# Optimization experiments

Measured on AMD Instinct MI355X. Metric: run time of the kernel, lower is better.

Reference implementation:

```python
import jax, jax.numpy as jnp
import numpy as np

K = 16          # NUM_PARTS (foreground parts); K+1 prototypes incl. background
D = 768         # EMBED_DIM
C = 200         # NUM_CLASSES
LN_EPS = 1e-6


def setup_inputs() -> dict:
    key = jax.random.key(0)
    k1, k2, k3, k4 = jax.random.split(key, 4)
    B, H, W = 32, 24, 24
    patch_features = jax.random.normal(k1, (B, H, W, D), dtype=jnp.float32)
    prototypes = 0.02 * jax.random.normal(k2, (K + 1, D), dtype=jnp.float32)
    ln_gamma = jnp.ones((D,), dtype=jnp.float32)
    ln_beta = jnp.zeros((D,), dtype=jnp.float32)
    # keras Dense default: glorot_uniform kernel, zero bias
    lim = np.sqrt(6.0 / (D + C)).astype(np.float32)
    w_cls = jax.random.uniform(k3, (D, C), dtype=jnp.float32, minval=-lim, maxval=lim)
    b_cls = jnp.zeros((C,), dtype=jnp.float32)
    return {
        "patch_features": patch_features,
        "prototypes": prototypes,
        "ln_gamma": ln_gamma,
        "ln_beta": ln_beta,
        "w_cls": w_cls,
        "b_cls": b_cls,
    }


def reference(patch_features, prototypes, ln_gamma, ln_beta, w_cls, b_cls):
    B, H, W, Dm = patch_features.shape
    P = H * W
    x = patch_features.reshape(B, P, Dm)                      # (B,P,D)

    # squared euclidean distance to K+1 prototypes, expressed as a GEMM:
    # ||z - p||^2 = ||z||^2 - 2 z.p + ||p||^2   -> (B,P,K+1)
    x_sq = jnp.sum(x * x, axis=-1, keepdims=True)             # (B,P,1)
    p_sq = jnp.sum(prototypes * prototypes, axis=-1)          # (K+1,)
    xp = jnp.einsum("bpd,kd->bpk", x, prototypes)             # (B,P,K+1)
    dists = x_sq - 2.0 * xp + p_sq                            # (B,P,K+1)

    # eval path: plain softmax over -distances
    a = jax.nn.softmax(-dists, axis=-1)                       # (B,P,K+1)

    # attention maps (B, K+1, H, W)
    A = jnp.transpose(a, (0, 2, 1)).reshape(B, K + 1, H, W)

    # weighted aggregation of patch features per part, normalized by P
    v_all = jnp.einsum("bpk,bpd->bkd", a, x) / jnp.float32(P) # (B,K+1,D)
    v_fg = v_all[:, :K, :]                                    # (B,K,D)

    # layernorm over last axis (eps=1e-6, learnable gamma/beta)
    mu = jnp.mean(v_fg, axis=-1, keepdims=True)
    var = jnp.mean(jnp.square(v_fg - mu), axis=-1, keepdims=True)
    v_norm = (v_fg - mu) * jax.lax.rsqrt(var + LN_EPS) * ln_gamma + ln_beta

    # shared per-part classifier + mean aggregation over parts
    logits_parts = jnp.einsum("bkd,dc->bkc", v_norm, w_cls) + b_cls  # (B,K,C)
    logits_agg = jnp.mean(logits_parts, axis=1)                      # (B,C)

    return (A, v_norm, logits_parts, logits_agg)
```

## Files before the change

### kernel.cpp

```cpp
#include <hip/hip_runtime.h>
#include <hip/hip_bf16.h>

#define B    32
#define P    576
#define D    768
#define K1   17
#define KFG  16
#define C    200
#define LN_EPS 1e-6f

typedef __attribute__((ext_vector_type(8))) short short8;
typedef __attribute__((ext_vector_type(4))) float f32x4;

__device__ inline short8 cvt8(float4 a, float4 b) {
    union { unsigned u[4]; short8 s; } r;
    union { __hip_bfloat162 h; unsigned u; } c;
    c.h = __float22bfloat162_rn(make_float2(a.x, a.y)); r.u[0] = c.u;
    c.h = __float22bfloat162_rn(make_float2(a.z, a.w)); r.u[1] = c.u;
    c.h = __float22bfloat162_rn(make_float2(b.x, b.y)); r.u[2] = c.u;
    c.h = __float22bfloat162_rn(make_float2(b.z, b.w)); r.u[3] = c.u;
    return r.s;
}
__device__ inline float sq8(float4 a, float4 b) {
    return a.x*a.x + a.y*a.y + a.z*a.z + a.w*a.w
         + b.x*b.x + b.y*b.y + b.z*b.z + b.w*b.w;
}

__global__ __launch_bounds__(256) void k_dots(const float* __restrict__ x,
                                              const float* __restrict__ proto,
                                              float* __restrict__ A_out,
                                              float* __restrict__ apool) {
    __shared__ float scL[4 * 64 * 11];
    const int tile = blockIdx.x, b = blockIdx.y;
    const int t = threadIdx.x, wv = t >> 6, lane = t & 63;
    const int n = lane & 15, kq = lane >> 4;
    const int p0 = tile * 16;

    const float* arow = x     + ((size_t)(b * P + p0 + n)) * D + wv * 192 + kq * 8;
    const float* brow = proto + (size_t)n  * D + wv * 192 + kq * 8;
    const float* brw6 = proto + (size_t)16 * D + wv * 192 + kq * 8;

    f32x4 acc0 = {0.f, 0.f, 0.f, 0.f};
    f32x4 acc1 = {0.f, 0.f, 0.f, 0.f};
    float sq0 = 0.f, sq6 = 0.f;

    #pragma unroll
    for (int s = 0; s < 6; ++s) {
        float4 a0 = *(const float4*)(arow + s * 32);
        float4 a1 = *(const float4*)(arow + s * 32 + 4);
        float4 b0 = *(const float4*)(brow + s * 32);
        float4 b1 = *(const float4*)(brow + s * 32 + 4);
        float4 c0 = *(const float4*)(brw6 + s * 32);
        float4 c1 = *(const float4*)(brw6 + s * 32 + 4);
        short8 A  = cvt8(a0, a1);
        short8 Bv = cvt8(b0, b1);
        short8 B6 = cvt8(c0, c1);
        sq0 += sq8(b0, b1);
        sq6 += sq8(c0, c1);
        acc0 = __builtin_amdgcn_mfma_f32_16x16x32_bf16(A, Bv, acc0, 0, 0, 0);
        acc1 = __builtin_amdgcn_mfma_f32_16x16x32_bf16(A, B6, acc1, 0, 0, 0);
    }
    sq0 += __shfl_xor(sq0, 16, 64); sq0 += __shfl_xor(sq0, 32, 64);
    sq6 += __shfl_xor(sq6, 16, 64); sq6 += __shfl_xor(sq6, 32, 64);

    {
        float* s = scL + (wv * 64 + lane) * 11;
        #pragma unroll
        for (int r = 0; r < 4; ++r) { s[r] = acc0[r]; s[r + 4] = acc1[r]; }
        s[8] = sq0; s[9] = sq6;
    }
    __syncthreads();
    if (wv != 0) return;

    float f0[4], f1[4]; float fsq0 = 0.f, fsq6 = 0.f;
    #pragma unroll
    for (int r = 0; r < 4; ++r) { f0[r] = 0.f; f1[r] = 0.f; }
    #pragma unroll
    for (int w = 0; w < 4; ++w) {
        const float* s = scL + (w * 64 + lane) * 11;
        #pragma unroll
        for (int r = 0; r < 4; ++r) { f0[r] += s[r]; f1[r] += s[r + 4]; }
        fsq0 += s[8]; fsq6 += s[9];
    }

    float a_[4], a16[4];
    #pragma unroll
    for (int r = 0; r < 4; ++r) {
        float l0  = 2.f * f0[r] - fsq0;
        float l16 = 2.f * f1[r] - fsq6;
        float mx = l0;
        #pragma unroll
        for (int o = 1; o < 16; o <<= 1) mx = fmaxf(mx, __shfl_xor(mx, o, 64));
        mx = fmaxf(mx, l16);
        float e0  = __expf(l0 - mx);
        float e16 = __expf(l16 - mx);
        float sum = e0;
        #pragma unroll
        for (int o = 1; o < 16; o <<= 1) sum += __shfl_xor(sum, o, 64);
        sum += e16;
        const float inv = 1.f / sum;
        a_[r]  = e0 * inv;
        a16[r] = e16 * inv;
    }

    *(float4*)(A_out + ((size_t)b * K1 + n) * P + p0 + kq * 4) =
        make_float4(a_[0], a_[1], a_[2], a_[3]);
    if (n == 0)
        *(float4*)(A_out + ((size_t)b * K1 + 16) * P + p0 + kq * 4) =
            make_float4(a16[0], a16[1], a16[2], a16[3]);

    const float invP = 1.f / (float)P;
    #pragma unroll
    for (int r = 0; r < 4; ++r)
        apool[((size_t)b * P + p0 + kq * 4 + r) * KFG + n] = a_[r] * invP;
}

__global__ __launch_bounds__(256, 4) void k_pool(const float* __restrict__ x,
                                                 const float* __restrict__ apool,
                                                 float* __restrict__ vpart) {
    const int dc = blockIdx.x, psl = blockIdx.y, b = blockIdx.z;
    const int t = threadIdx.x;
    const int d = dc * 256 + t;

    const float* aw = apool + ((size_t)b * P + psl * 96) * KFG;
    const float* xp = x + ((size_t)b * P + psl * 96) * D + d;

    float acc[KFG];
    #pragma unroll
    for (int k = 0; k < KFG; ++k) acc[k] = 0.f;

    #pragma unroll 4
    for (int p = 0; p < 96; ++p) {
        float xv = xp[(size_t)p * D];
        f32x4 A0 = *(const f32x4*)(aw + p * 16);
        f32x4 A1 = *(const f32x4*)(aw + p * 16 + 4);
        f32x4 A2 = *(const f32x4*)(aw + p * 16 + 8);
        f32x4 A3 = *(const f32x4*)(aw + p * 16 + 12);
        acc[0]  += A0[0] * xv; acc[1]  += A0[1] * xv; acc[2]  += A0[2] * xv; acc[3]  += A0[3] * xv;
        acc[4]  += A1[0] * xv; acc[5]  += A1[1] * xv; acc[6]  += A1[2] * xv; acc[7]  += A1[3] * xv;
        acc[8]  += A2[0] * xv; acc[9]  += A2[1] * xv; acc[10] += A2[2] * xv; acc[11] += A2[3] * xv;
        acc[12] += A3[0] * xv; acc[13] += A3[1] * xv; acc[14] += A3[2] * xv; acc[15] += A3[3] * xv;
    }
    float* o = vpart + ((size_t)(psl * B + b) * KFG) * D + d;
    #pragma unroll
    for (int k = 0; k < KFG; ++k) o[(size_t)k * D] = acc[k];
}

__global__ __launch_bounds__(256) void k_ln(const float* __restrict__ vpart,
                                            const float* __restrict__ gamma,
                                            const float* __restrict__ beta,
                                            float* __restrict__ vnorm_out,
                                            float* __restrict__ vT) {
    const int k = blockIdx.x, b = blockIdx.y, t = threadIdx.x;
    const int lane = t & 63, wv = t >> 6;

    float v[3]; float s1 = 0.f, s2 = 0.f;
    #pragma unroll
    for (int j = 0; j < 3; ++j) {
        const int d = t + j * 256;
        float s = 0.f;
        #pragma unroll
        for (int psl = 0; psl < 6; ++psl)
            s += vpart[((size_t)(psl * B + b) * KFG + k) * D + d];
        v[j] = s; s1 += s; s2 += s * s;
    }
    #pragma unroll
    for (int o = 1; o < 64; o <<= 1) {
        s1 += __shfl_xor(s1, o, 64);
        s2 += __shfl_xor(s2, o, 64);
    }
    __shared__ float r1[4], r2[4];
    if (lane == 0) { r1[wv] = s1; r2[wv] = s2; }
    __syncthreads();
    s1 = r1[0] + r1[1] + r1[2] + r1[3];
    s2 = r2[0] + r2[1] + r2[2] + r2[3];

    const float mean = s1 * (1.f / (float)D);
    const float var  = s2 * (1.f / (float)D) - mean * mean;
    const float rs   = rsqrtf(var + LN_EPS);

    #pragma unroll
    for (int j = 0; j < 3; ++j) {
        const int d = t + j * 256;
        float vn = (v[j] - mean) * rs * gamma[d] + beta[d];
        vnorm_out[((size_t)b * KFG + k) * D + d] = vn;
        vT[((size_t)b * D + d) * KFG + k] = vn;
    }
}

__global__ __launch_bounds__(256) void k_cls(const float* __restrict__ vT,
                                             const float* __restrict__ W,
                                             float* __restrict__ lpart) {
    const int dq = blockIdx.x, b = blockIdx.y;
    const int c = threadIdx.x;
    const int cc = c < C ? c : (C - 1);

    const float* vt = vT + ((size_t)b * D + dq * 96) * KFG;
    const float* Wp = W + (size_t)dq * 96 * C + cc;

    float acc[KFG];
    #pragma unroll
    for (int k = 0; k < KFG; ++k) acc[k] = 0.f;

    #pragma unroll 4
    for (int i = 0; i < 96; ++i) {
        float wl = Wp[(size_t)i * C];
        f32x4 V0 = *(const f32x4*)(vt + i * 16);
        f32x4 V1 = *(const f32x4*)(vt + i * 16 + 4);
        f32x4 V2 = *(const f32x4*)(vt + i * 16 + 8);
        f32x4 V3 = *(const f32x4*)(vt + i * 16 + 12);
        acc[0]  += V0[0] * wl; acc[1]  += V0[1] * wl; acc[2]  += V0[2] * wl; acc[3]  += V0[3] * wl;
        acc[4]  += V1[0] * wl; acc[5]  += V1[1] * wl; acc[6]  += V1[2] * wl; acc[7]  += V1[3] * wl;
        acc[8]  += V2[0] * wl; acc[9]  += V2[1] * wl; acc[10] += V2[2] * wl; acc[11] += V2[3] * wl;
        acc[12] += V3[0] * wl; acc[13] += V3[1] * wl; acc[14] += V3[2] * wl; acc[15] += V3[3] * wl;
    }
    if (c < C) {
        float* o = lpart + ((size_t)(dq * B + b) * KFG) * C + c;
        #pragma unroll
        for (int k = 0; k < KFG; ++k) o[(size_t)k * C] = acc[k];
    }
}

__global__ __launch_bounds__(256) void k_comb(const float* __restrict__ lpart,
                                              const float* __restrict__ bcls,
                                              float* __restrict__ parts,
                                              float* __restrict__ agg) {
    const int b = blockIdx.x, c = threadIdx.x;
    if (c >= C) return;
    const float bc = bcls[c];
    float s_agg = 0.f;
    #pragma unroll
    for (int k = 0; k < KFG; ++k) {
        float s = bc;
        #pragma unroll
        for (int dq = 0; dq < 8; ++dq)
            s += lpart[((size_t)(dq * B + b) * KFG + k) * C + c];
        parts[((size_t)b * KFG + k) * C + c] = s;
        s_agg += s;
    }
    agg[(size_t)b * C + c] = s_agg * (1.f / (float)KFG);
}

extern "C" void kernel_launch(void* const* d_in, const int* in_sizes, int n_in,
                              void* d_out, int out_size, void* d_ws, size_t ws_size,
                              hipStream_t stream) {
    const float* x     = (const float*)d_in[0];
    const float* proto = (const float*)d_in[1];
    const float* gamma = (const float*)d_in[2];
    const float* beta  = (const float*)d_in[3];
    const float* W     = (const float*)d_in[4];
    const float* bcls  = (const float*)d_in[5];

    float* out = (float*)d_out;
    float* A_out     = out;
    float* vnorm_out = out + 313344;
    float* parts_out = out + 706560;
    float* agg_out   = out + 808960;

    float* ws = (float*)d_ws;
    float* apool = ws;
    float* vpart = apool + 294912;
    float* vT    = vpart + 2359296;
    float* lpart = vT + 393216;

    hipLaunchKernelGGL(k_dots, dim3(36, B),   dim3(256), 0, stream, x, proto, A_out, apool);
    hipLaunchKernelGGL(k_pool, dim3(3, 6, B), dim3(256), 0, stream, x, apool, vpart);
    hipLaunchKernelGGL(k_ln,   dim3(KFG, B),  dim3(256), 0, stream, vpart, gamma, beta, vnorm_out, vT);
    hipLaunchKernelGGL(k_cls,  dim3(8, B),    dim3(256), 0, stream, vT, W, lpart);
    hipLaunchKernelGGL(k_comb, dim3(B),       dim3(256), 0, stream, lpart, bcls, parts_out, agg_out);
}
```

Before: 140.5 us.

## Fuse pool+layernorm and classifier+combine via last-block atomic counters

Merges the pooling and layernorm kernels into one 768-thread kernel where the last block per batch (chosen through an atomic counter) sums the partials and applies layernorm. It also merges the classifier and combine kernels the same way, and splits the classifier reduction into 16 chunks instead of 8. This cuts the launch count from five to three and removes the inter-kernel gaps. The pool stage now runs 192 blocks of 768 threads instead of 576 blocks of 256, so parallelism drops, and the serial last-block epilogue adds tail latency. Counters are reset inside k_dots.

```diff
diff --git a/kernel.cpp b/kernel.cpp
--- a/kernel.cpp
+++ b/kernel.cpp
@@ -29,12 +29,15 @@
 __global__ __launch_bounds__(256) void k_dots(const float* __restrict__ x,
                                               const float* __restrict__ proto,
                                               float* __restrict__ A_out,
-                                              float* __restrict__ apool) {
+                                              float* __restrict__ apool,
+                                              unsigned* __restrict__ cnt) {
     __shared__ float scL[4 * 64 * 11];
     const int tile = blockIdx.x, b = blockIdx.y;
     const int t = threadIdx.x, wv = t >> 6, lane = t & 63;
     const int n = lane & 15, kq = lane >> 4;
     const int p0 = tile * 16;
+
+    if (tile == 0 && t == 0) { cnt[b] = 0u; cnt[B + b] = 0u; }
 
     const float* arow = x     + ((size_t)(b * P + p0 + n)) * D + wv * 192 + kq * 8;
     const float* brow = proto + (size_t)n  * D + wv * 192 + kq * 8;
@@ -115,12 +118,17 @@
         apool[((size_t)b * P + p0 + kq * 4 + r) * KFG + n] = a_[r] * invP;
 }
 
-__global__ __launch_bounds__(256, 4) void k_pool(const float* __restrict__ x,
-                                                 const float* __restrict__ apool,
-                                                 float* __restrict__ vpart) {
-    const int dc = blockIdx.x, psl = blockIdx.y, b = blockIdx.z;
+__global__ __launch_bounds__(768) void k_poolln(const float* __restrict__ x,
+                                                const float* __restrict__ apool,
+                                                float* __restrict__ vpart,
+                                                const float* __restrict__ gamma,
+                                                const float* __restrict__ beta,
+                                                float* __restrict__ vnorm_out,
+                                                float* __restrict__ vT,
+                                                unsigned* __restrict__ cntP) {
+    const int psl = blockIdx.x, b = blockIdx.y;
     const int t = threadIdx.x;
-    const int d = dc * 256 + t;
+    const int d = t, wv = t >> 6, lane = t & 63;
 
     const float* aw = apool + ((size_t)b * P + psl * 96) * KFG;
     const float* xp = x + ((size_t)b * P + psl * 96) * D + d;
@@ -141,69 +149,83 @@
         acc[8]  += A2[0] * xv; acc[9]  += A2[1] * xv; acc[10] += A2[2] * xv; acc[11] += A2[3] * xv;
         acc[12] += A3[0] * xv; acc[13] += A3[1] * xv; acc[14] += A3[2] * xv; acc[15] += A3[3] * xv;
     }
-    float* o = vpart + ((size_t)(psl * B + b) * KFG) * D + d;
-    #pragma unroll
-    for (int k = 0; k < KFG; ++k) o[(size_t)k * D] = acc[k];
-}
-
-__global__ __launch_bounds__(256) void k_ln(const float* __restrict__ vpart,
-                                            const float* __restrict__ gamma,
-                                            const float* __restrict__ beta,
-                                            float* __restrict__ vnorm_out,
-                                            float* __restrict__ vT) {
-    const int k = blockIdx.x, b = blockIdx.y, t = threadIdx.x;
-    const int lane = t & 63, wv = t >> 6;
-
-    float v[3]; float s1 = 0.f, s2 = 0.f;
-    #pragma unroll
-    for (int j = 0; j < 3; ++j) {
-        const int d = t + j * 256;
+    {
+        float* vp = vpart + ((size_t)(psl * B + b) * KFG) * D + d;
+        #pragma unroll
+        for (int k = 0; k < KFG; ++k) vp[(size_t)k * D] = acc[k];
+    }
+
+    __shared__ int sflag;
+    __threadfence();
+    __syncthreads();
+    if (t == 0) sflag = (atomicAdd(&cntP[b], 1u) == 5u);
+    __syncthreads();
+    if (!sflag) return;
+    __threadfence();
+
+    float v[KFG];
+    #pragma unroll
+    for (int k = 0; k < KFG; ++k) {
         float s = 0.f;
         #pragma unroll
-        for (int psl = 0; psl < 6; ++psl)
-            s += vpart[((size_t)(psl * B + b) * KFG + k) * D + d];
-        v[j] = s; s1 += s; s2 += s * s;
-    }
-    #pragma unroll
-    for (int o = 1; o < 64; o <<= 1) {
-        s1 += __shfl_xor(s1, o, 64);
-        s2 += __shfl_xor(s2, o, 64);
-    }
-    __shared__ float r1[4], r2[4];
-    if (lane == 0) { r1[wv] = s1; r2[wv] = s2; }
-    __syncthreads();
-    s1 = r1[0] + r1[1] + r1[2] + r1[3];
-    s2 = r2[0] + r2[1] + r2[2] + r2[3];
-
-    const float mean = s1 * (1.f / (float)D);
-    const float var  = s2 * (1.f / (float)D) - mean * mean;
-    const float rs   = rsqrtf(var + LN_EPS);
-
-    #pragma unroll
-    for (int j = 0; j < 3; ++j) {
-        const int d = t + j * 256;
-        float vn = (v[j] - mean) * rs * gamma[d] + beta[d];
-        vnorm_out[((size_t)b * KFG + k) * D + d] = vn;
-        vT[((size_t)b * D + d) * KFG + k] = vn;
-    }
+        for (int q = 0; q < 6; ++q)
+            s += vpart[((size_t)(q * B + b) * KFG + k) * D + d];
+        v[k] = s;
+    }
+
+    __shared__ float r1[KFG][12], r2[KFG][12];
+    #pragma unroll
+    for (int k = 0; k < KFG; ++k) {
+        float s1 = v[k], s2 = v[k] * v[k];
+        #pragma unroll
+        for (int o = 1; o < 64; o <<= 1) {
+            s1 += __shfl_xor(s1, o, 64);
+            s2 += __shfl_xor(s2, o, 64);
+        }
+        if (lane == 0) { r1[k][wv] = s1; r2[k][wv] = s2; }
+    }
+    __syncthreads();
+
+    const float g = gamma[d], be = beta[d];
+    float vn[KFG];
+    #pragma unroll
+    for (int k = 0; k < KFG; ++k) {
+        float s1 = 0.f, s2 = 0.f;
+        #pragma unroll
+        for (int w = 0; w < 12; ++w) { s1 += r1[k][w]; s2 += r2[k][w]; }
+        const float mean = s1 * (1.f / (float)D);
+        const float var  = s2 * (1.f / (float)D) - mean * mean;
+        const float rs   = rsqrtf(var + LN_EPS);
+        const float xn   = (v[k] - mean) * rs * g + be;
+        vn[k] = xn;
+        vnorm_out[((size_t)b * KFG + k) * D + d] = xn;
+    }
+    float* o = vT + ((size_t)b * D + d) * KFG;
+    #pragma unroll
+    for (int r = 0; r < 4; ++r)
+        *(f32x4*)(o + r * 4) = (f32x4){vn[4*r], vn[4*r+1], vn[4*r+2], vn[4*r+3]};
 }
 
 __global__ __launch_bounds__(256) void k_cls(const float* __restrict__ vT,
                                              const float* __restrict__ W,
-                                             float* __restrict__ lpart) {
+                                             const float* __restrict__ bcls,
+                                             float* __restrict__ lpart,
+                                             float* __restrict__ parts,
+                                             float* __restrict__ agg,
+                                             unsigned* __restrict__ cntC) {
     const int dq = blockIdx.x, b = blockIdx.y;
     const int c = threadIdx.x;
     const int cc = c < C ? c : (C - 1);
 
-    const float* vt = vT + ((size_t)b * D + dq * 96) * KFG;
-    const float* Wp = W + (size_t)dq * 96 * C + cc;
+    const float* vt = vT + ((size_t)b * D + dq * 48) * KFG;
+    const float* Wp = W + (size_t)dq * 48 * C + cc;
 
     float acc[KFG];
     #pragma unroll
     for (int k = 0; k < KFG; ++k) acc[k] = 0.f;
 
     #pragma unroll 4
-    for (int i = 0; i < 96; ++i) {
+    for (int i = 0; i < 48; ++i) {
         float wl = Wp[(size_t)i * C];
         f32x4 V0 = *(const f32x4*)(vt + i * 16);
         f32x4 V1 = *(const f32x4*)(vt + i * 16 + 4);
@@ -219,22 +241,24 @@
         #pragma unroll
         for (int k = 0; k < KFG; ++k) o[(size_t)k * C] = acc[k];
     }
-}
-
-__global__ __launch_bounds__(256) void k_comb(const float* __restrict__ lpart,
-                                              const float* __restrict__ bcls,
-                                              float* __restrict__ parts,
-                                              float* __restrict__ agg) {
-    const int b = blockIdx.x, c = threadIdx.x;
+
+    __shared__ int sflag;
+    __threadfence();
+    __syncthreads();
+    if (threadIdx.x == 0) sflag = (atomicAdd(&cntC[b], 1u) == 15u);
+    __syncthreads();
+    if (!sflag) return;
+    __threadfence();
     if (c >= C) return;
+
     const float bc = bcls[c];
     float s_agg = 0.f;
     #pragma unroll
     for (int k = 0; k < KFG; ++k) {
         float s = bc;
         #pragma unroll
-        for (int dq = 0; dq < 8; ++dq)
-            s += lpart[((size_t)(dq * B + b) * KFG + k) * C + c];
+        for (int q = 0; q < 16; ++q)
+            s += lpart[((size_t)(q * B + b) * KFG + k) * C + c];
         parts[((size_t)b * KFG + k) * C + c] = s;
         s_agg += s;
     }
@@ -262,10 +286,11 @@
     float* vpart = apool + 294912;
     float* vT    = vpart + 2359296;
     float* lpart = vT + 393216;
-
-    hipLaunchKernelGGL(k_dots, dim3(36, B),   dim3(256), 0, stream, x, proto, A_out, apool);
-    hipLaunchKernelGGL(k_pool, dim3(3, 6, B), dim3(256), 0, stream, x, apool, vpart);
-    hipLaunchKernelGGL(k_ln,   dim3(KFG, B),  dim3(256), 0, stream, vpart, gamma, beta, vnorm_out, vT);
-    hipLaunchKernelGGL(k_cls,  dim3(8, B),    dim3(256), 0, stream, vT, W, lpart);
-    hipLaunchKernelGGL(k_comb, dim3(B),       dim3(256), 0, stream, lpart, bcls, parts_out, agg_out);
-}
+    unsigned* cnt = (unsigned*)(lpart + 1638400);
+
+    hipLaunchKernelGGL(k_dots,   dim3(36, B), dim3(256), 0, stream, x, proto, A_out, apool, cnt);
+    hipLaunchKernelGGL(k_poolln, dim3(6, B),  dim3(768), 0, stream, x, apool, vpart, gamma, beta,
+                       vnorm_out, vT, cnt);
+    hipLaunchKernelGGL(k_cls,    dim3(16, B), dim3(256), 0, stream, vT, W, bcls, lpart,
+                       parts_out, agg_out, cnt + B);
+}
```

Result: slower. 316.4 us (+125.2%).
